# Optimization experiments

Hardware: AMD Instinct MI355X
Metric: run time of the kernel (lower is better)

## Reference

```python
import jax, jax.numpy as jnp
import numpy as np

VOCAB, E, H, B, T = 32000, 256, 256, 512, 128
PAD = 0
EPS = 1e-12


def setup_inputs() -> dict:
    key = jax.random.key(0)
    ks = jax.random.split(key, 20)
    captions = jax.random.randint(ks[0], (B, T), 0, VOCAB)
    emb = jax.random.normal(ks[1], (VOCAB, E), dtype=jnp.float32) * 0.02
    emb = emb.at[PAD].set(0.0)  # padding_idx row is zero in nn.Embedding
    s_in = 1.0 / np.sqrt(E)
    s_h = 1.0 / np.sqrt(H)
    d = {"captions": captions, "emb": emb}
    names = ["i", "f", "o", "c"]
    for j, n in enumerate(names):
        d[f"W_{n}"] = jax.random.uniform(ks[2 + 4 * j], (E, H), minval=-s_in, maxval=s_in)
        d[f"bW_{n}"] = jax.random.uniform(ks[3 + 4 * j], (H,), minval=-s_in, maxval=s_in)
        d[f"U_{n}"] = jax.random.uniform(ks[4 + 4 * j], (H, H), minval=-s_h, maxval=s_h)
        d[f"bU_{n}"] = jax.random.uniform(ks[5 + 4 * j], (H,), minval=-s_h, maxval=s_h)
    d["fc_w"] = jax.random.uniform(ks[18], (H, E), minval=-s_h, maxval=s_h)
    d["fc_b"] = jax.random.uniform(ks[19], (E,), minval=-s_h, maxval=s_h)
    return d


def _lstm_forward(captions, emb,
                  W_i, bW_i, U_i, bU_i,
                  W_f, bW_f, U_f, bU_f,
                  W_o, bW_o, U_o, bU_o,
                  W_c, bW_c, U_c, bU_c,
                  fc_w, fc_b):
    x = emb[captions]  # [B,T,E]
    mask = (captions != PAD).astype(x.dtype)[..., None]  # [B,T,1]
    # Precompute input-side gate projections for all timesteps (batched GEMM).
    xi = jnp.einsum("bte,eh->bth", x, W_i) + bW_i
    xf = jnp.einsum("bte,eh->bth", x, W_f) + bW_f
    xo = jnp.einsum("bte,eh->bth", x, W_o) + bW_o
    xg = jnp.einsum("bte,eh->bth", x, W_c) + bW_c
    # time-major for scan: [T,B,H]
    xs = (jnp.swapaxes(xi, 0, 1), jnp.swapaxes(xf, 0, 1),
          jnp.swapaxes(xo, 0, 1), jnp.swapaxes(xg, 0, 1),
          jnp.swapaxes(mask, 0, 1))
    h0 = jnp.zeros((captions.shape[0], U_i.shape[0]), dtype=x.dtype)
    c0 = jnp.zeros_like(h0)

    def step(carry, inp):
        h, c = carry
        xi_t, xf_t, xo_t, xg_t, m = inp
        g = jnp.tanh(xg_t + h @ U_c + bU_c)
        i = jax.nn.sigmoid(xi_t + h @ U_i + bU_i)
        f = jax.nn.sigmoid(xf_t + h @ U_f + bU_f)
        o = jax.nn.sigmoid(xo_t + h @ U_o + bU_o)
        c = i * g + f * c
        c = m * c + (1.0 - m) * jax.lax.stop_gradient(c)
        h = o * jnp.tanh(c)
        h = m * h + (1.0 - m) * jax.lax.stop_gradient(h)
        return (h, c), None

    (h, _), _ = jax.lax.scan(step, (h0, c0), xs)
    out = h @ fc_w + fc_b  # [B,E]
    norm = jnp.maximum(jnp.linalg.norm(out, axis=1, keepdims=True), EPS)
    return out / norm


def reference(captions, emb,
              W_i, bW_i, U_i, bU_i,
              W_f, bW_f, U_f, bU_f,
              W_o, bW_o, U_o, bU_o,
              W_c, bW_c, U_c, bU_c,
              fc_w, fc_b):
    return _lstm_forward(captions, emb,
                         W_i, bW_i, U_i, bU_i,
                         W_f, bW_f, U_f, bU_f,
                         W_o, bW_o, U_o, bU_o,
                         W_c, bW_c, U_c, bU_c,
                         fc_w, fc_b)
```

## Files before the change

### kernel.cpp

```cpp
#include <hip/hip_runtime.h>
#include <stdint.h>

typedef unsigned short ushort_t;
typedef __attribute__((ext_vector_type(8))) short bf8_t;
typedef __attribute__((ext_vector_type(4))) float f4_t;
typedef __attribute__((ext_vector_type(4))) unsigned short us4_t;

#define TT 128

__device__ __forceinline__ ushort_t f2bf(float f) {
  uint32_t u = __builtin_bit_cast(uint32_t, f);
  u += 0x7fffu + ((u >> 16) & 1u);
  return (ushort_t)(u >> 16);
}
__device__ __forceinline__ float bf2f(ushort_t h) {
  uint32_t u = ((uint32_t)h) << 16;
  return __builtin_bit_cast(float, u);
}
__device__ __forceinline__ float sigm(float x) {
  return __builtin_amdgcn_rcpf(1.f + __expf(-x));
}
__device__ __forceinline__ float tanh_f(float x) {
  return 1.f - 2.f * __builtin_amdgcn_rcpf(1.f + __expf(2.f * x));
}

__device__ __forceinline__ void x_store16(void* p, bf8_t v) {
  asm volatile("global_store_dwordx4 %0, %1, off sc0 sc1" :: "v"(p), "v"(v) : "memory");
}
__device__ __forceinline__ void x_store_flag_byte(void* p, unsigned v) {
  asm volatile("global_store_byte %0, %1, off sc0 sc1" :: "v"(p), "v"(v) : "memory");
}
__device__ __forceinline__ unsigned x_load_flag(const void* p) {
  unsigned v;
  asm volatile("global_load_dword %0, %1, off sc0 sc1\n\ts_waitcnt vmcnt(0)"
               : "=v"(v) : "v"(p) : "memory");
  return v;
}
__device__ __forceinline__ void x_load4_issue(const void* p, bf8_t f[4]) {
  asm volatile(
      "global_load_dwordx4 %0, %4, off sc0 sc1\n\t"
      "global_load_dwordx4 %1, %4, off offset:1024 sc0 sc1\n\t"
      "global_load_dwordx4 %2, %4, off offset:2048 sc0 sc1\n\t"
      "global_load_dwordx4 %3, %4, off offset:3072 sc0 sc1"
      : "=&v"(f[0]), "=&v"(f[1]), "=&v"(f[2]), "=&v"(f[3]) : "v"(p) : "memory");
}

__global__ void k_pack_w(const float* W0, const float* W1, const float* W2, const float* W3,
                         ushort_t* __restrict__ o) {
  int idx = blockIdx.x * 256 + threadIdx.x;
  int n = idx >> 8, k = idx & 255;
  int g = n & 3, j = n >> 2;
  const float* Wg = g == 0 ? W0 : g == 1 ? W1 : g == 2 ? W2 : W3;
  o[(size_t)n * 256 + k] = f2bf(Wg[k * 256 + j]);
}

__global__ void k_pack_u2(const float* U0, const float* U1, const float* U2, const float* U3,
                          ushort_t* __restrict__ o) {
  int idx = blockIdx.x * 256 + threadIdx.x;
  int lane = idx & 63, g = (idx >> 6) & 3, ktS = (idx >> 8) & 7,
      w = (idx >> 11) & 7, q = (idx >> 14) & 1;
  const float* Ug = g == 0 ? U0 : g == 1 ? U1 : g == 2 ? U2 : U3;
  int ktG = (ktS + 4 * q) & 7;
  int col = q * 128 + w * 16 + (lane & 15);
  int kb = ktG * 32 + (lane >> 4) * 8;
#pragma unroll
  for (int e = 0; e < 8; ++e)
    o[(size_t)idx * 8 + e] = f2bf(Ug[(size_t)(kb + e) * 256 + col]);
}

__global__ void k_bias(const float* a0, const float* a1, const float* a2, const float* a3,
                       const float* b0, const float* b1, const float* b2, const float* b3,
                       float* __restrict__ o) {
  int n = blockIdx.x * 256 + threadIdx.x;
  int g = n & 3, j = n >> 2;
  const float* pa = g == 0 ? a0 : g == 1 ? a1 : g == 2 ? a2 : a3;
  const float* pb = g == 0 ? b0 : g == 1 ? b1 : g == 2 ? b2 : b3;
  o[n] = pa[j] + pb[j];
}

__global__ __launch_bounds__(256) void k1g_gemm(const float* __restrict__ A,
                                                const ushort_t* __restrict__ Bm,
                                                const float* __restrict__ bias,
                                                const int* __restrict__ cap,
                                                ushort_t* __restrict__ Pg) {
  __shared__ ushort_t Al[128 * 32];
  __shared__ ushort_t Bl[128 * 32];
  const int tid = threadIdx.x;
  const int lane = tid & 63;
  const int w = tid >> 6;
  const int mt = blockIdx.x >> 3;
  const int nt = blockIdx.x & 7;
  const int m0 = mt * 128, n0 = nt * 128;
  const int qr = (w >> 1) * 64, qc = (w & 1) * 64;

  f4_t acc[4][4];
#pragma unroll
  for (int i = 0; i < 4; ++i)
#pragma unroll
    for (int j = 0; j < 4; ++j) acc[i][j] = f4_t{0.f, 0.f, 0.f, 0.f};

  const int r0 = tid >> 2, s0 = tid & 3;
  const int r1 = 64 + r0;
  const int t0 = cap[m0 + r0];
  const int t1 = cap[m0 + r1];

  for (int k0 = 0; k0 < 256; k0 += 32) {
    float4 a00 = *(const float4*)(A + (size_t)t0 * 256 + k0 + s0 * 8);
    float4 a01 = *(const float4*)(A + (size_t)t0 * 256 + k0 + s0 * 8 + 4);
    float4 a10 = *(const float4*)(A + (size_t)t1 * 256 + k0 + s0 * 8);
    float4 a11 = *(const float4*)(A + (size_t)t1 * 256 + k0 + s0 * 8 + 4);
    bf8_t b0 = *(const bf8_t*)(Bm + (size_t)(n0 + r0) * 256 + k0 + s0 * 8);
    bf8_t b1 = *(const bf8_t*)(Bm + (size_t)(n0 + r1) * 256 + k0 + s0 * 8);
    bf8_t pa0, pa1;
    pa0[0] = (short)f2bf(a00.x); pa0[1] = (short)f2bf(a00.y);
    pa0[2] = (short)f2bf(a00.z); pa0[3] = (short)f2bf(a00.w);
    pa0[4] = (short)f2bf(a01.x); pa0[5] = (short)f2bf(a01.y);
    pa0[6] = (short)f2bf(a01.z); pa0[7] = (short)f2bf(a01.w);
    pa1[0] = (short)f2bf(a10.x); pa1[1] = (short)f2bf(a10.y);
    pa1[2] = (short)f2bf(a10.z); pa1[3] = (short)f2bf(a10.w);
    pa1[4] = (short)f2bf(a11.x); pa1[5] = (short)f2bf(a11.y);
    pa1[6] = (short)f2bf(a11.z); pa1[7] = (short)f2bf(a11.w);
    __syncthreads();
    *(bf8_t*)(Al + (size_t)tid * 8) = pa0;
    *(bf8_t*)(Al + (size_t)(256 + tid) * 8) = pa1;
    *(bf8_t*)(Bl + (size_t)tid * 8) = b0;
    *(bf8_t*)(Bl + (size_t)(256 + tid) * 8) = b1;
    __syncthreads();
    bf8_t af[4], bfr[4];
#pragma unroll
    for (int i = 0; i < 4; ++i) {
      af[i]  = *(const bf8_t*)(Al + (qr + i * 16 + (lane & 15)) * 32 + (lane >> 4) * 8);
      bfr[i] = *(const bf8_t*)(Bl + (qc + i * 16 + (lane & 15)) * 32 + (lane >> 4) * 8);
    }
#pragma unroll
    for (int i = 0; i < 4; ++i)
#pragma unroll
      for (int j = 0; j < 4; ++j)
        acc[i][j] = __builtin_amdgcn_mfma_f32_16x16x32_bf16(af[i], bfr[j], acc[i][j], 0, 0, 0);
  }
#pragma unroll
  for (int i = 0; i < 4; ++i)
#pragma unroll
    for (int j = 0; j < 4; ++j)
#pragma unroll
      for (int r = 0; r < 4; ++r) {
        int row = m0 + qr + i * 16 + (lane >> 4) * 4 + r;
        int col = n0 + qc + j * 16 + (lane & 15);
        Pg[(size_t)row * 1024 + col] = f2bf(acc[i][j][r] + bias[col]);
      }
}

__global__ __launch_bounds__(512, 2) void k_scan4(
    const ushort_t* __restrict__ Pg, const ushort_t* __restrict__ UPJ,
    float* __restrict__ hfin, char* __restrict__ pbuf, char* __restrict__ flags) {
  __shared__ ushort_t hlds[2][2048];
  const int blk = blockIdx.x;
  const int pair = blk >> 1, q = blk & 1;
  const int tid = threadIdx.x, lane = tid & 63, w = tid >> 6;
  const int l15 = lane & 15, l16 = lane >> 4;
  const int jc = q * 128 + w * 16 + l15;
  const int row0 = pair * 16 + l16 * 4;

  bf8_t u[8][4];
  {
    const ushort_t* ub = UPJ + (size_t)(q * 8 + w) * 32 * 512 + (size_t)lane * 8;
#pragma unroll
    for (int kt = 0; kt < 8; ++kt)
#pragma unroll
      for (int g = 0; g < 4; ++g)
        u[kt][g] = *(const bf8_t*)(ub + (kt * 4 + g) * 512);
  }

  const ushort_t* pg[4];
#pragma unroll
  for (int r = 0; r < 4; ++r)
    pg[r] = Pg + ((size_t)(row0 + r) * TT) * 1024 + jc * 4;

  float c[4] = {0.f, 0.f, 0.f, 0.f};
  f4_t acc[4];
#pragma unroll
  for (int g = 0; g < 4; ++g) acc[g] = f4_t{0.f, 0.f, 0.f, 0.f};

  us4_t pf[4];
#pragma unroll
  for (int r = 0; r < 4; ++r) { pf[r] = *(const us4_t*)pg[r]; pg[r] += 1024; }

  const int wfrag = (w >> 1) * 4 + (w & 1) * 2 + (l15 >> 3);
  const int wbase = wfrag * 128 + l16 * 32 + (l15 & 7);
  char* pairbuf = pbuf + (size_t)pair * 16384;
  char* fown = flags + (size_t)(pair * 2 + q) * TT * 4;
  const char* fpar = flags + (size_t)(pair * 2 + (1 - q)) * TT * 4;

  for (int t = 0; t < TT; ++t) {
    float hv[4];
#pragma unroll
    for (int r = 0; r < 4; ++r) {
      float pi = acc[0][r] + bf2f(pf[r].x);
      float pF = acc[1][r] + bf2f(pf[r].y);
      float po = acc[2][r] + bf2f(pf[r].z);
      float pg_ = acc[3][r] + bf2f(pf[r].w);
      float ig = sigm(pi), fg = sigm(pF), og = sigm(po), gg = tanh_f(pg_);
      float cn = fmaf(fg, c[r], ig * gg);
      c[r] = cn;
      hv[r] = og * tanh_f(cn);
    }
    if (t == TT - 1) {
#pragma unroll
      for (int r = 0; r < 4; ++r)
        hfin[(size_t)(row0 + r) * 256 + jc] = hv[r];
      break;
    }
    const int par = t & 1;
    {
      ushort_t* hb = &hlds[par][0];
#pragma unroll
      for (int r = 0; r < 4; ++r) hb[wbase + r * 8] = f2bf(hv[r]);
    }
    __syncthreads();
    if (tid < 256) {
      bf8_t v = *(const bf8_t*)(&hlds[par][tid * 8]);
      x_store16(pairbuf + par * 8192 + q * 4096 + tid * 16, v);
      asm volatile("s_waitcnt vmcnt(0)" ::: "memory");
      if (lane == 0) x_store_flag_byte(fown + t * 4 + w, 1u);
    }
    {
      unsigned fv = x_load_flag(fpar + t * 4);
      while (fv != 0x01010101u) {
        __builtin_amdgcn_s_sleep(1);
        fv = x_load_flag(fpar + t * 4);
      }
    }
#pragma unroll
    for (int g = 0; g < 4; ++g) acc[g] = f4_t{0.f, 0.f, 0.f, 0.f};
    bf8_t paf[4];
    x_load4_issue(pairbuf + par * 8192 + (1 - q) * 4096 + (l16 * 16 + l15) * 16, paf);
#pragma unroll
    for (int r = 0; r < 4; ++r) { pf[r] = *(const us4_t*)pg[r]; pg[r] += 1024; }
#pragma unroll
    for (int kt = 0; kt < 4; ++kt) {
      bf8_t afk = *(const bf8_t*)(&hlds[par][((kt * 4 + l16) * 16 + l15) * 8]);
#pragma unroll
      for (int g = 0; g < 4; ++g)
        acc[g] = __builtin_amdgcn_mfma_f32_16x16x32_bf16(afk, u[kt][g], acc[g], 0, 0, 0);
    }
    asm volatile("s_waitcnt vmcnt(4)" ::: "memory");
    __builtin_amdgcn_sched_barrier(0);
#pragma unroll
    for (int kt = 0; kt < 4; ++kt)
#pragma unroll
      for (int g = 0; g < 4; ++g)
        acc[g] = __builtin_amdgcn_mfma_f32_16x16x32_bf16(paf[kt], u[4 + kt][g], acc[g], 0, 0, 0);
  }
}

__global__ __launch_bounds__(256) void k3_fc(const float* __restrict__ hfin,
                                             const float* __restrict__ fcw,
                                             const float* __restrict__ fcb,
                                             float* __restrict__ out) {
  __shared__ float hrow[256];
  __shared__ float red[4];
  const int b = blockIdx.x, j = threadIdx.x;
  hrow[j] = hfin[(size_t)b * 256 + j];
  __syncthreads();
  float acc = fcb[j];
#pragma unroll 4
  for (int k = 0; k < 256; ++k) acc = fmaf(hrow[k], fcw[(size_t)k * 256 + j], acc);
  float ss = acc * acc;
#pragma unroll
  for (int o = 32; o > 0; o >>= 1) ss += __shfl_down(ss, o);
  if ((j & 63) == 0) red[j >> 6] = ss;
  __syncthreads();
  float tot = red[0] + red[1] + red[2] + red[3];
  float nrm = fmaxf(sqrtf(tot), 1e-12f);
  out[(size_t)b * 256 + j] = acc / nrm;
}

extern "C" void kernel_launch(void* const* d_in, const int* in_sizes, int n_in,
                              void* d_out, int out_size, void* d_ws, size_t ws_size,
                              hipStream_t stream) {
  const int* captions = (const int*)d_in[0];
  const float* emb = (const float*)d_in[1];
  const float *W[4], *bW[4], *U[4], *bU[4];
  for (int g = 0; g < 4; ++g) {
    W[g]  = (const float*)d_in[2 + 4 * g];
    bW[g] = (const float*)d_in[3 + 4 * g];
    U[g]  = (const float*)d_in[4 + 4 * g];
    bU[g] = (const float*)d_in[5 + 4 * g];
  }
  const float* fcw = (const float*)d_in[18];
  const float* fcb = (const float*)d_in[19];
  float* out = (float*)d_out;
  char* ws = (char*)d_ws;

  ushort_t* Pg    = (ushort_t*)(ws);
  ushort_t* WT    = (ushort_t*)(ws + 134217728);
  ushort_t* UPJ2  = (ushort_t*)(ws + 134742016);
  float*    bias  = (float*)   (ws + 135266304);
  float*    hfin  = (float*)   (ws + 135270400);
  char*     pbuf  = (char*)    (ws + 135794688);
  char*     flags = (char*)    (ws + 136318976);

  hipMemsetAsync(flags, 0, 32768, stream);
  k_pack_w<<<1024, 256, 0, stream>>>(W[0], W[1], W[2], W[3], WT);
  k_pack_u2<<<128, 256, 0, stream>>>(U[0], U[1], U[2], U[3], UPJ2);
  k_bias<<<4, 256, 0, stream>>>(bW[0], bW[1], bW[2], bW[3],
                                bU[0], bU[1], bU[2], bU[3], bias);
  k1g_gemm<<<4096, 256, 0, stream>>>(emb, WT, bias, captions, Pg);
  k_scan4<<<64, 512, 0, stream>>>(Pg, UPJ2, hfin, pbuf, flags);
  k3_fc<<<512, 256, 0, stream>>>(hfin, fcw, fcb, out);
}
```

Before: 441.4 us.

## Project the vocabulary table once and gather token projections inside the scan

The input GEMM now projects the whole embedding table (32000 rows) through the gate weights instead of the B*T gathered token rows, writing a per-vocab projection table. The recurrent scan kernel then loads the captions and gathers each timestep's gate preactivations from this table by token id, with the token ids prefetched two steps ahead and the wait count adjusted to match. This cuts GEMM rows roughly in half and shrinks the workspace. In exchange the scan does dependent, scattered gathers on its critical path.

```diff
diff --git a/kernel.cpp b/kernel.cpp
--- a/kernel.cpp
+++ b/kernel.cpp
@@ -78,11 +78,10 @@
   o[n] = pa[j] + pb[j];
 }
 
-__global__ __launch_bounds__(256) void k1g_gemm(const float* __restrict__ A,
-                                                const ushort_t* __restrict__ Bm,
-                                                const float* __restrict__ bias,
-                                                const int* __restrict__ cap,
-                                                ushort_t* __restrict__ Pg) {
+__global__ __launch_bounds__(256) void k1_gemm(const float* __restrict__ A,
+                                               const ushort_t* __restrict__ Bm,
+                                               const float* __restrict__ bias,
+                                               ushort_t* __restrict__ P) {
   __shared__ ushort_t Al[128 * 32];
   __shared__ ushort_t Bl[128 * 32];
   const int tid = threadIdx.x;
@@ -101,14 +100,12 @@
 
   const int r0 = tid >> 2, s0 = tid & 3;
   const int r1 = 64 + r0;
-  const int t0 = cap[m0 + r0];
-  const int t1 = cap[m0 + r1];
 
   for (int k0 = 0; k0 < 256; k0 += 32) {
-    float4 a00 = *(const float4*)(A + (size_t)t0 * 256 + k0 + s0 * 8);
-    float4 a01 = *(const float4*)(A + (size_t)t0 * 256 + k0 + s0 * 8 + 4);
-    float4 a10 = *(const float4*)(A + (size_t)t1 * 256 + k0 + s0 * 8);
-    float4 a11 = *(const float4*)(A + (size_t)t1 * 256 + k0 + s0 * 8 + 4);
+    float4 a00 = *(const float4*)(A + (size_t)(m0 + r0) * 256 + k0 + s0 * 8);
+    float4 a01 = *(const float4*)(A + (size_t)(m0 + r0) * 256 + k0 + s0 * 8 + 4);
+    float4 a10 = *(const float4*)(A + (size_t)(m0 + r1) * 256 + k0 + s0 * 8);
+    float4 a11 = *(const float4*)(A + (size_t)(m0 + r1) * 256 + k0 + s0 * 8 + 4);
     bf8_t b0 = *(const bf8_t*)(Bm + (size_t)(n0 + r0) * 256 + k0 + s0 * 8);
     bf8_t b1 = *(const bf8_t*)(Bm + (size_t)(n0 + r1) * 256 + k0 + s0 * 8);
     bf8_t pa0, pa1;
@@ -146,13 +143,14 @@
       for (int r = 0; r < 4; ++r) {
         int row = m0 + qr + i * 16 + (lane >> 4) * 4 + r;
         int col = n0 + qc + j * 16 + (lane & 15);
-        Pg[(size_t)row * 1024 + col] = f2bf(acc[i][j][r] + bias[col]);
+        P[(size_t)row * 1024 + col] = f2bf(acc[i][j][r] + bias[col]);
       }
 }
 
-__global__ __launch_bounds__(512, 2) void k_scan4(
-    const ushort_t* __restrict__ Pg, const ushort_t* __restrict__ UPJ,
-    float* __restrict__ hfin, char* __restrict__ pbuf, char* __restrict__ flags) {
+__global__ __launch_bounds__(512, 2) void k_scan5(
+    const ushort_t* __restrict__ P, const ushort_t* __restrict__ UPJ,
+    const int* __restrict__ cap, float* __restrict__ hfin,
+    char* __restrict__ pbuf, char* __restrict__ flags) {
   __shared__ ushort_t hlds[2][2048];
   const int blk = blockIdx.x;
   const int pair = blk >> 1, q = blk & 1;
@@ -171,19 +169,20 @@
         u[kt][g] = *(const bf8_t*)(ub + (kt * 4 + g) * 512);
   }
 
-  const ushort_t* pg[4];
-#pragma unroll
-  for (int r = 0; r < 4; ++r)
-    pg[r] = Pg + ((size_t)(row0 + r) * TT) * 1024 + jc * 4;
-
   float c[4] = {0.f, 0.f, 0.f, 0.f};
   f4_t acc[4];
 #pragma unroll
   for (int g = 0; g < 4; ++g) acc[g] = f4_t{0.f, 0.f, 0.f, 0.f};
 
+  int tok[4];
+#pragma unroll
+  for (int r = 0; r < 4; ++r) tok[r] = cap[(row0 + r) * TT];
   us4_t pf[4];
 #pragma unroll
-  for (int r = 0; r < 4; ++r) { pf[r] = *(const us4_t*)pg[r]; pg[r] += 1024; }
+  for (int r = 0; r < 4; ++r)
+    pf[r] = *(const us4_t*)(P + (size_t)tok[r] * 1024 + jc * 4);
+#pragma unroll
+  for (int r = 0; r < 4; ++r) tok[r] = cap[(row0 + r) * TT + 1];
 
   const int wfrag = (w >> 1) * 4 + (w & 1) * 2 + (l15 >> 3);
   const int wbase = wfrag * 128 + l16 * 32 + (l15 & 7);
@@ -235,7 +234,13 @@
     bf8_t paf[4];
     x_load4_issue(pairbuf + par * 8192 + (1 - q) * 4096 + (l16 * 16 + l15) * 16, paf);
 #pragma unroll
-    for (int r = 0; r < 4; ++r) { pf[r] = *(const us4_t*)pg[r]; pg[r] += 1024; }
+    for (int r = 0; r < 4; ++r)
+      pf[r] = *(const us4_t*)(P + (size_t)tok[r] * 1024 + jc * 4);
+    {
+      const int t2 = (t + 2 < TT) ? t + 2 : TT - 1;
+#pragma unroll
+      for (int r = 0; r < 4; ++r) tok[r] = cap[(row0 + r) * TT + t2];
+    }
 #pragma unroll
     for (int kt = 0; kt < 4; ++kt) {
       bf8_t afk = *(const bf8_t*)(&hlds[par][((kt * 4 + l16) * 16 + l15) * 8]);
@@ -243,7 +248,7 @@
       for (int g = 0; g < 4; ++g)
         acc[g] = __builtin_amdgcn_mfma_f32_16x16x32_bf16(afk, u[kt][g], acc[g], 0, 0, 0);
     }
-    asm volatile("s_waitcnt vmcnt(4)" ::: "memory");
+    asm volatile("s_waitcnt vmcnt(8)" ::: "memory");
     __builtin_amdgcn_sched_barrier(0);
 #pragma unroll
     for (int kt = 0; kt < 4; ++kt)
@@ -292,20 +297,20 @@
   float* out = (float*)d_out;
   char* ws = (char*)d_ws;
 
-  ushort_t* Pg    = (ushort_t*)(ws);
-  ushort_t* WT    = (ushort_t*)(ws + 134217728);
-  ushort_t* UPJ2  = (ushort_t*)(ws + 134742016);
-  float*    bias  = (float*)   (ws + 135266304);
-  float*    hfin  = (float*)   (ws + 135270400);
-  char*     pbuf  = (char*)    (ws + 135794688);
-  char*     flags = (char*)    (ws + 136318976);
+  ushort_t* P     = (ushort_t*)(ws);
+  ushort_t* WT    = (ushort_t*)(ws + 65536000);
+  ushort_t* UPJ2  = (ushort_t*)(ws + 66060288);
+  float*    bias  = (float*)   (ws + 66584576);
+  float*    hfin  = (float*)   (ws + 66588672);
+  char*     pbuf  = (char*)    (ws + 67112960);
+  char*     flags = (char*)    (ws + 67637248);
 
   hipMemsetAsync(flags, 0, 32768, stream);
   k_pack_w<<<1024, 256, 0, stream>>>(W[0], W[1], W[2], W[3], WT);
   k_pack_u2<<<128, 256, 0, stream>>>(U[0], U[1], U[2], U[3], UPJ2);
   k_bias<<<4, 256, 0, stream>>>(bW[0], bW[1], bW[2], bW[3],
                                 bU[0], bU[1], bU[2], bU[3], bias);
-  k1g_gemm<<<4096, 256, 0, stream>>>(emb, WT, bias, captions, Pg);
-  k_scan4<<<64, 512, 0, stream>>>(Pg, UPJ2, hfin, pbuf, flags);
+  k1_gemm<<<2000, 256, 0, stream>>>(emb, WT, bias, P);
+  k_scan5<<<64, 512, 0, stream>>>(P, UPJ2, captions, hfin, pbuf, flags);
   k3_fc<<<512, 256, 0, stream>>>(hfin, fcw, fcb, out);
 }
```

Result: faster. 413.6 us, median of 2 (-6.3%).
